# Performance work log

Measured on AMD Instinct MI355X. Metric: run time of the kernel, lower is better.

The kernel has to match this reference:

```python
import jax, jax.numpy as jnp
import numpy as np

B, N, D, H = 8, 2048, 256, 4
HD = D // H


def setup_inputs() -> dict:
    key = jax.random.key(0)
    ks = jax.random.split(key, 12)
    s = 1.0 / np.sqrt(D)
    inp = {
        "node_features": jax.random.normal(ks[0], (B, N, D), dtype=jnp.float32),
        "causal_mask": jnp.tril(jnp.ones((N, N), dtype=jnp.float32)),
        "Wq": jax.random.normal(ks[1], (D, D), dtype=jnp.float32) * s,
        "bq": jnp.zeros((D,), dtype=jnp.float32),
        "Wk": jax.random.normal(ks[2], (D, D), dtype=jnp.float32) * s,
        "bk": jnp.zeros((D,), dtype=jnp.float32),
        "Wv": jax.random.normal(ks[3], (D, D), dtype=jnp.float32) * s,
        "bv": jnp.zeros((D,), dtype=jnp.float32),
        "Wo": jax.random.normal(ks[4], (D, D), dtype=jnp.float32) * s,
        "bo": jnp.zeros((D,), dtype=jnp.float32),
        "Wu": jax.random.normal(ks[5], (2 * D, D), dtype=jnp.float32) * (1.0 / np.sqrt(2 * D)),
        "bu": jnp.zeros((D,), dtype=jnp.float32),
    }
    return inp


def reference(node_features, causal_mask, Wq, bq, Wk, bk, Wv, bv, Wo, bo, Wu, bu):
    # node_features: [B, N, D]; causal_mask: [N, N] (1 = keep, 0 = masked)
    x = node_features
    # project and split heads -> [B, H, N, HD]
    def heads(w, b):
        return (x @ w + b).reshape(B, N, H, HD).transpose(0, 2, 1, 3)
    q, k, v = heads(Wq, bq), heads(Wk, bk), heads(Wv, bv)
    scale = 1.0 / np.sqrt(HD).astype(np.float32)
    scores = jnp.einsum("bhnd,bhmd->bhnm", q, k) * scale  # [B, H, N, N]
    scores = jnp.where(causal_mask > 0, scores, jnp.float32(-1e9))
    attn = jax.nn.softmax(scores, axis=-1)
    ctx = jnp.einsum("bhnm,bhmd->bhnd", attn, v)  # [B, H, N, HD]
    messages = ctx.transpose(0, 2, 1, 3).reshape(B, N, D) @ Wo + bo  # [B, N, D]
    combined = jnp.concatenate([x, messages], axis=-1)  # [B, N, 2D]
    updated = jax.nn.relu(combined @ Wu + bu)  # [B, N, D]  (dropout = identity in eval)
    return updated
```

## Files before the change

kernel.cpp:

```cpp
#include <hip/hip_runtime.h>
#include <math.h>

constexpr int B  = 8;
constexpr int N  = 2048;
constexpr int D  = 256;
constexpr int H  = 4;
constexpr int HD = 64;
constexpr int MTOT = B * N;

typedef __attribute__((ext_vector_type(8))) short  short8;
typedef __attribute__((ext_vector_type(4))) float  floatx4;
typedef unsigned short ushort_t;

#define QSCALE 0.1803368801111204f

__device__ __forceinline__ unsigned short f2bf(float f) {
    unsigned u = __float_as_uint(f);
    u += 0x7fffu + ((u >> 16) & 1u);
    return (unsigned short)(u >> 16);
}

__device__ __forceinline__ void gl_lds16(const ushort_t* g, ushort_t* l) {
    __builtin_amdgcn_global_load_lds(
        (const __attribute__((address_space(1))) void*)g,
        (__attribute__((address_space(3))) void*)l, 16, 0, 0);
}

__global__ __launch_bounds__(256) void prep(
    const float* __restrict__ x,
    const float* __restrict__ Wq, const float* __restrict__ Wk,
    const float* __restrict__ Wv, const float* __restrict__ Wo,
    const float* __restrict__ Wu,
    ushort_t* __restrict__ xb,
    ushort_t* __restrict__ wqkvt, ushort_t* __restrict__ wot,
    ushort_t* __restrict__ wut)
{
    __shared__ float Ls[64][65];
    const int bx = blockIdx.x;
    const int t  = threadIdx.x;

    if (bx < 2048) {
        int idx = (bx * 256 + t) * 8;
        float4 a = *(const float4*)(x + idx);
        float4 b = *(const float4*)(x + idx + 4);
        ushort_t o[8] = {f2bf(a.x), f2bf(a.y), f2bf(a.z), f2bf(a.w),
                         f2bf(b.x), f2bf(b.y), f2bf(b.z), f2bf(b.w)};
        *(short8*)(xb + idx) = *(const short8*)o;
        return;
    }

    const int e = bx - 2048;
    const int z = e >> 5;
    const int kt = (e & 31) >> 2;
    const int nt = e & 3;
    const float* src; ushort_t* dst; int K;
    if      (z == 0) { src = Wq; dst = wqkvt;          K = 256; }
    else if (z == 1) { src = Wk; dst = wqkvt + 65536;  K = 256; }
    else if (z == 2) { src = Wv; dst = wqkvt + 131072; K = 256; }
    else if (z == 3) { src = Wo; dst = wot;            K = 256; }
    else             { src = Wu; dst = wut;            K = 512; }
    if (kt * 64 >= K) return;
    #pragma unroll
    for (int i = 0; i < 16; i++) {
        int ee = t + i * 256, r = ee >> 6, c = ee & 63;
        Ls[r][c] = src[(size_t)(kt * 64 + r) * 256 + nt * 64 + c];
    }
    __syncthreads();
    #pragma unroll
    for (int i = 0; i < 16; i++) {
        int ee = t + i * 256, r = ee >> 6, c = ee & 63;
        dst[(size_t)(nt * 64 + r) * K + kt * 64 + c] = f2bf(Ls[c][r]);
    }
}

__global__ __launch_bounds__(256) void qkv_gemm(
    const ushort_t* __restrict__ xb, const ushort_t* __restrict__ wqkvt,
    const float* __restrict__ bq, const float* __restrict__ bk,
    const float* __restrict__ bv,
    ushort_t* __restrict__ q, ushort_t* __restrict__ kout,
    ushort_t* __restrict__ vt)
{
    __shared__ ushort_t SH[16896];
    ushort_t* As = SH;
    ushort_t* Bs = SH + 8192;

    const int t = threadIdx.x, w = t >> 6, lane = t & 63;
    const int quad = lane >> 4, l16 = lane & 15;
    const int bx = blockIdx.x;
    const int col0 = bx * 128, row0 = blockIdx.y * 128;
    const int wr = (w >> 1) * 64, wc = (w & 1) * 64;

    floatx4 acc[4][4] = {};

    for (int k0 = 0; k0 < 256; k0 += 64) {
        __syncthreads();
        #pragma unroll
        for (int i = 0; i < 4; i++) {
            int e = t + (i << 8);
            int r = e >> 3, c8 = (e & 7) << 3;
            gl_lds16(xb    + (size_t)(row0 + r) * 256 + k0 + c8, &As[e * 8]);
            gl_lds16(wqkvt + (size_t)(col0 + r) * 256 + k0 + c8, &Bs[e * 8]);
        }
        __syncthreads();

        #pragma unroll
        for (int kk = 0; kk < 64; kk += 32) {
            short8 af[4], bf[4];
            #pragma unroll
            for (int i = 0; i < 4; i++)
                af[i] = *(const short8*)&As[(wr + i * 16 + l16) * 64 + kk + quad * 8];
            #pragma unroll
            for (int j = 0; j < 4; j++)
                bf[j] = *(const short8*)&Bs[(wc + j * 16 + l16) * 64 + kk + quad * 8];
            #pragma unroll
            for (int i = 0; i < 4; i++)
                #pragma unroll
                for (int j = 0; j < 4; j++)
                    acc[i][j] = __builtin_amdgcn_mfma_f32_16x16x32_bf16(
                        af[i], bf[j], acc[i][j], 0, 0, 0);
        }
    }

    const int kind = bx >> 1;
    const float* bias = (kind == 0) ? bq : (kind == 1 ? bk : bv);
    const float scl  = (kind == 0) ? QSCALE : 1.0f;
    __syncthreads();
    ushort_t (*Ts)[132] = (ushort_t(*)[132])SH;
    #pragma unroll
    for (int j = 0; j < 4; j++) {
        int cl = wc + j * 16 + l16;
        float bsv = bias[(bx & 1) * 128 + cl];
        #pragma unroll
        for (int i = 0; i < 4; i++) {
            #pragma unroll
            for (int r = 0; r < 4; r++) {
                int ml = wr + i * 16 + quad * 4 + r;
                ushort_t bvv = f2bf((acc[i][j][r] + bsv) * scl);
                if (kind < 2) Ts[ml][cl] = bvv;
                else          Ts[cl][ml] = bvv;
            }
        }
    }
    __syncthreads();

    const int b = row0 >> 11, n0 = row0 & (N - 1);
    #pragma unroll
    for (int i = 0; i < 8; i++) {
        int id = t + (i << 8);
        int rr = id >> 4, c8 = (id & 15) << 3;
        short8 val = *(const short8*)&Ts[rr][c8];
        if (kind < 2) {
            int cg = (bx & 1) * 128 + c8;
            int h = cg >> 6, hd = cg & 63;
            ushort_t* dst = (kind == 0) ? q : kout;
            *(short8*)&dst[(((size_t)(b * H + h)) * N + n0 + rr) * HD + hd] = val;
        } else {
            int cg = (bx & 1) * 128 + rr;
            int h = cg >> 6, hd = cg & 63;
            *(short8*)&vt[(((size_t)(b * H + h)) * HD + hd) * N + n0 + c8] = val;
        }
    }
}

__global__ __launch_bounds__(512) void attn_mfma(
    const ushort_t* __restrict__ q,
    const ushort_t* __restrict__ k,
    const ushort_t* __restrict__ vt,
    ushort_t* __restrict__ ctxb)
{
    __shared__ ushort_t Ks [128][68];
    __shared__ ushort_t Vts[64][132];
    __shared__ ushort_t Ps [8][16][36];

    const int t    = threadIdx.x;
    const int w    = t >> 6;
    const int lane = t & 63;
    const int quad = lane >> 4;
    const int l16  = lane & 15;
    const int bh   = blockIdx.x;
    const int b    = bh >> 2, h = bh & 3;
    const int by   = blockIdx.y;
    const int grp  = w >> 2;
    const int qt   = grp ? by : (31 - by);
    const int qbase = qt * 64;
    const int rowb  = qbase + (w & 3) * 16;

    const ushort_t* qp = q  + (size_t)bh * N * HD;
    const ushort_t* kp = k  + (size_t)bh * N * HD;
    const ushort_t* vp = vt + (size_t)bh * HD * N;

    short8 qf0, qf1;
    {
        const ushort_t* qrow = qp + (size_t)(rowb + l16) * HD + quad * 8;
        qf0 = *(const short8*)(qrow);
        qf1 = *(const short8*)(qrow + 32);
    }

    floatx4 acc_o[4] = {};
    float plsum[4] = {};

    const int nkt_self = (qt >> 1) + 1;
    const int nkt_max  = ((31 - by) >> 1) + 1;

    for (int kt = 0; kt < nkt_max; kt++) {
        const int kbase = kt * 128;
        __syncthreads();

        #pragma unroll
        for (int i = 0; i < 2; i++) {
            int e  = t + (i << 9);
            int kr = e >> 3, kc = (e & 7) << 3;
            *(short8*)&Ks[kr][kc] =
                *(const short8*)(kp + (size_t)(kbase + kr) * HD + kc);
            int vr = e >> 4, vc = (e & 15) << 3;
            *(short8*)&Vts[vr][vc] =
                *(const short8*)(vp + (size_t)vr * N + kbase + vc);
        }
        __syncthreads();

        if (kt >= nkt_self) continue;

        int rem = rowb + 15 - kbase;
        int nch = (rem < 0) ? 0 : ((rem >> 5) + 1);
        if (nch > 4) nch = 4;

        for (int ch = 0; ch < nch; ch++) {
            #pragma unroll
            for (int c2 = 0; c2 < 2; c2++) {
                const int ct = ch * 2 + c2;
                short8 kf0 = *(const short8*)&Ks[ct * 16 + l16][quad * 8];
                short8 kf1 = *(const short8*)&Ks[ct * 16 + l16][32 + quad * 8];
                floatx4 z = {0.0f, 0.0f, 0.0f, 0.0f};
                floatx4 s = __builtin_amdgcn_mfma_f32_16x16x32_bf16(qf0, kf0, z, 0, 0, 0);
                s         = __builtin_amdgcn_mfma_f32_16x16x32_bf16(qf1, kf1, s, 0, 0, 0);
                const bool partial = (kbase + ct * 16 + 15) > rowb;
                if (partial) {
                    const int keyg = kbase + ct * 16 + l16;
                    #pragma unroll
                    for (int r = 0; r < 4; r++) {
                        float sv = s[r];
                        if (keyg > rowb + quad * 4 + r) sv = -3.0e38f;
                        float pv = __builtin_amdgcn_exp2f(sv);
                        plsum[r] += pv;
                        Ps[w][quad * 4 + r][c2 * 16 + l16] = f2bf(pv);
                    }
                } else {
                    #pragma unroll
                    for (int r = 0; r < 4; r++) {
                        float pv = __builtin_amdgcn_exp2f(s[r]);
                        plsum[r] += pv;
                        Ps[w][quad * 4 + r][c2 * 16 + l16] = f2bf(pv);
                    }
                }
            }
            short8 pf = *(const short8*)&Ps[w][l16][quad * 8];
            #pragma unroll
            for (int nt = 0; nt < 4; nt++) {
                short8 vf = *(const short8*)&Vts[nt * 16 + l16][ch * 32 + quad * 8];
                acc_o[nt] = __builtin_amdgcn_mfma_f32_16x16x32_bf16(pf, vf, acc_o[nt], 0, 0, 0);
            }
        }
    }

    #pragma unroll
    for (int r = 0; r < 4; r++) {
        float l = plsum[r];
        l += __shfl_xor(l, 1);
        l += __shfl_xor(l, 2);
        l += __shfl_xor(l, 4);
        l += __shfl_xor(l, 8);
        float inv = 1.0f / l;
        int   n   = rowb + quad * 4 + r;
        #pragma unroll
        for (int nt = 0; nt < 4; nt++) {
            ctxb[((size_t)(b * N + n)) * D + h * HD + nt * 16 + l16] =
                f2bf(acc_o[nt][r] * inv);
        }
    }
}

__global__ __launch_bounds__(256) void tail_k(
    const ushort_t* __restrict__ ctxb, const ushort_t* __restrict__ xb,
    const ushort_t* __restrict__ wot,  const ushort_t* __restrict__ wut,
    const float* __restrict__ bo, const float* __restrict__ bu,
    float* __restrict__ out)
{
    __shared__ ushort_t As1[32 * 64];
    __shared__ ushort_t Bs [256 * 64];
    __shared__ ushort_t msgS[32][260];

    const int t = threadIdx.x, w = t >> 6, lane = t & 63;
    const int quad = lane >> 4, l16 = lane & 15;
    const int row0 = blockIdx.x * 32;
    const int wc = w * 64;

    floatx4 acc1[2][4] = {};
    for (int k0 = 0; k0 < 256; k0 += 64) {
        __syncthreads();
        {
            int r = t >> 3, c8 = (t & 7) << 3;
            gl_lds16(ctxb + (size_t)(row0 + r) * 256 + k0 + c8, &As1[t * 8]);
        }
        #pragma unroll
        for (int i = 0; i < 8; i++) {
            int e = t + (i << 8);
            int nr = e >> 3, c8 = (e & 7) << 3;
            gl_lds16(wot + (size_t)nr * 256 + k0 + c8, &Bs[e * 8]);
        }
        __syncthreads();

        #pragma unroll
        for (int kk = 0; kk < 64; kk += 32) {
            short8 af[2], bf[4];
            #pragma unroll
            for (int i = 0; i < 2; i++)
                af[i] = *(const short8*)&As1[(i * 16 + l16) * 64 + kk + quad * 8];
            #pragma unroll
            for (int j = 0; j < 4; j++)
                bf[j] = *(const short8*)&Bs[(wc + j * 16 + l16) * 64 + kk + quad * 8];
            #pragma unroll
            for (int i = 0; i < 2; i++)
                #pragma unroll
                for (int j = 0; j < 4; j++)
                    acc1[i][j] = __builtin_amdgcn_mfma_f32_16x16x32_bf16(
                        af[i], bf[j], acc1[i][j], 0, 0, 0);
        }
    }
    #pragma unroll
    for (int j = 0; j < 4; j++) {
        int col = wc + j * 16 + l16;
        float bsv = bo[col];
        #pragma unroll
        for (int i = 0; i < 2; i++)
            #pragma unroll
            for (int r = 0; r < 4; r++)
                msgS[i * 16 + quad * 4 + r][col] = f2bf(acc1[i][j][r] + bsv);
    }

    floatx4 acc2[2][4] = {};
    for (int k0 = 0; k0 < 512; k0 += 64) {
        const bool xpart = (k0 < 256);
        __syncthreads();
        if (xpart) {
            int r = t >> 3, c8 = (t & 7) << 3;
            gl_lds16(xb + (size_t)(row0 + r) * 256 + k0 + c8, &As1[t * 8]);
        }
        #pragma unroll
        for (int i = 0; i < 8; i++) {
            int e = t + (i << 8);
            int nr = e >> 3, c8 = (e & 7) << 3;
            gl_lds16(wut + (size_t)nr * 512 + k0 + c8, &Bs[e * 8]);
        }
        __syncthreads();

        #pragma unroll
        for (int kk = 0; kk < 64; kk += 32) {
            short8 af[2], bf[4];
            #pragma unroll
            for (int i = 0; i < 2; i++) {
                if (xpart)
                    af[i] = *(const short8*)&As1[(i * 16 + l16) * 64 + kk + quad * 8];
                else
                    af[i] = *(const short8*)&msgS[i * 16 + l16][(k0 - 256) + kk + quad * 8];
            }
            #pragma unroll
            for (int j = 0; j < 4; j++)
                bf[j] = *(const short8*)&Bs[(wc + j * 16 + l16) * 64 + kk + quad * 8];
            #pragma unroll
            for (int i = 0; i < 2; i++)
                #pragma unroll
                for (int j = 0; j < 4; j++)
                    acc2[i][j] = __builtin_amdgcn_mfma_f32_16x16x32_bf16(
                        af[i], bf[j], acc2[i][j], 0, 0, 0);
        }
    }

    #pragma unroll
    for (int j = 0; j < 4; j++) {
        int col = wc + j * 16 + l16;
        float bsv = bu[col];
        #pragma unroll
        for (int i = 0; i < 2; i++) {
            #pragma unroll
            for (int r = 0; r < 4; r++) {
                int m = row0 + i * 16 + quad * 4 + r;
                out[(size_t)m * 256 + col] = fmaxf(acc2[i][j][r] + bsv, 0.0f);
            }
        }
    }
}

extern "C" void kernel_launch(void* const* d_in, const int* in_sizes, int n_in,
                              void* d_out, int out_size, void* d_ws, size_t ws_size,
                              hipStream_t stream)
{
    const float* x  = (const float*)d_in[0];
    const float* Wq = (const float*)d_in[2];
    const float* bq = (const float*)d_in[3];
    const float* Wk = (const float*)d_in[4];
    const float* bk = (const float*)d_in[5];
    const float* Wv = (const float*)d_in[6];
    const float* bv = (const float*)d_in[7];
    const float* Wo = (const float*)d_in[8];
    const float* bo = (const float*)d_in[9];
    const float* Wu = (const float*)d_in[10];
    const float* bu = (const float*)d_in[11];
    float* out = (float*)d_out;

    const size_t SZ = (size_t)MTOT * D;
    ushort_t* xb    = (ushort_t*)d_ws;
    ushort_t* qb    = xb    + SZ;
    ushort_t* kb    = qb    + SZ;
    ushort_t* vbt   = kb    + SZ;
    ushort_t* ctxb  = vbt   + SZ;
    ushort_t* wqkvt = ctxb  + SZ;
    ushort_t* wot   = wqkvt + 196608;
    ushort_t* wut   = wot   + 65536;

    prep<<<2208, 256, 0, stream>>>(x, Wq, Wk, Wv, Wo, Wu,
                                   xb, wqkvt, wot, wut);

    qkv_gemm<<<dim3(6, 128), 256, 0, stream>>>(xb, wqkvt, bq, bk, bv,
                                               qb, kb, vbt);

    attn_mfma<<<dim3(32, 16), 512, 0, stream>>>(qb, kb, vbt, ctxb);

    tail_k<<<512, 256, 0, stream>>>(ctxb, xb, wot, wut, bo, bu, out);
}
```

Before: 178.7 us.

## Fold Wo into Wu so the tail becomes a single fused GEMM

Precomputes Wo·Wu_bottom and bo·Wu_bottom+bu in the prep kernel, so the tail runs one K=512 GEMM over [x, ctx] instead of two chained GEMMs. This removes the Wo projection GEMM over all tokens (about a third of the tail FLOPs) and lets the tail use a 2D tile grid. Separately, the P-to-bf16 conversion in attention switches from round-to-nearest to truncation to save ALU work. The fold changes rounding, because the product is computed in fp32 and then stored as bf16, and truncation adds a small bias to the P values.

```diff
diff --git a/kernel.cpp b/kernel.cpp
--- a/kernel.cpp
+++ b/kernel.cpp
@@ -20,6 +20,10 @@
     return (unsigned short)(u >> 16);
 }
 
+__device__ __forceinline__ unsigned short f2bf_t(float f) {
+    return (unsigned short)(__float_as_uint(f) >> 16);
+}
+
 __device__ __forceinline__ void gl_lds16(const ushort_t* g, ushort_t* l) {
     __builtin_amdgcn_global_load_lds(
         (const __attribute__((address_space(1))) void*)g,
@@ -31,9 +35,10 @@
     const float* __restrict__ Wq, const float* __restrict__ Wk,
     const float* __restrict__ Wv, const float* __restrict__ Wo,
     const float* __restrict__ Wu,
+    const float* __restrict__ bo, const float* __restrict__ bu,
     ushort_t* __restrict__ xb,
-    ushort_t* __restrict__ wqkvt, ushort_t* __restrict__ wot,
-    ushort_t* __restrict__ wut)
+    ushort_t* __restrict__ wqkvt, ushort_t* __restrict__ wut,
+    float* __restrict__ b2)
 {
     __shared__ float Ls[64][65];
     const int bx = blockIdx.x;
@@ -49,27 +54,78 @@
         return;
     }
 
-    const int e = bx - 2048;
-    const int z = e >> 5;
-    const int kt = (e & 31) >> 2;
-    const int nt = e & 3;
-    const float* src; ushort_t* dst; int K;
-    if      (z == 0) { src = Wq; dst = wqkvt;          K = 256; }
-    else if (z == 1) { src = Wk; dst = wqkvt + 65536;  K = 256; }
-    else if (z == 2) { src = Wv; dst = wqkvt + 131072; K = 256; }
-    else if (z == 3) { src = Wo; dst = wot;            K = 256; }
-    else             { src = Wu; dst = wut;            K = 512; }
-    if (kt * 64 >= K) return;
-    #pragma unroll
-    for (int i = 0; i < 16; i++) {
-        int ee = t + i * 256, r = ee >> 6, c = ee & 63;
-        Ls[r][c] = src[(size_t)(kt * 64 + r) * 256 + nt * 64 + c];
-    }
-    __syncthreads();
-    #pragma unroll
-    for (int i = 0; i < 16; i++) {
-        int ee = t + i * 256, r = ee >> 6, c = ee & 63;
-        dst[(size_t)(nt * 64 + r) * K + kt * 64 + c] = f2bf(Ls[c][r]);
+    if (bx < 2112) {
+        const int e  = bx - 2048;
+        const int zz = e >> 4;
+        const int kt = (e >> 2) & 3;
+        const int nt = e & 3;
+        const float* src; ushort_t* dst; int K;
+        if      (zz == 0) { src = Wq; dst = wqkvt;          K = 256; }
+        else if (zz == 1) { src = Wk; dst = wqkvt + 65536;  K = 256; }
+        else if (zz == 2) { src = Wv; dst = wqkvt + 131072; K = 256; }
+        else              { src = Wu; dst = wut;            K = 512; }
+        #pragma unroll
+        for (int i = 0; i < 16; i++) {
+            int ee = t + i * 256, r = ee >> 6, c = ee & 63;
+            Ls[r][c] = src[(size_t)(kt * 64 + r) * 256 + nt * 64 + c];
+        }
+        __syncthreads();
+        #pragma unroll
+        for (int i = 0; i < 16; i++) {
+            int ee = t + i * 256, r = ee >> 6, c = ee & 63;
+            dst[(size_t)(nt * 64 + r) * K + kt * 64 + c] = f2bf(Ls[c][r]);
+        }
+        return;
+    }
+
+    if (bx < 2128) {
+        float* As2 = &Ls[0][0];
+        float* Ws2 = As2 + 16 * 65;
+        const int e2   = bx - 2112;
+        const int row0 = (e2 >> 2) * 64;
+        const int col0 = (e2 & 3) * 64;
+        const int r0 = (t >> 4) << 2;
+        const int c0 = (t & 15) << 2;
+        float acc[4][4] = {};
+        for (int k0 = 0; k0 < 256; k0 += 16) {
+            __syncthreads();
+            #pragma unroll
+            for (int i = 0; i < 4; i++) {
+                int ee = t + (i << 8);
+                int rr = ee >> 4, kk = ee & 15;
+                As2[kk * 65 + rr] = Wo[(size_t)(row0 + rr) * 256 + k0 + kk];
+                int kk2 = ee >> 6, cc = ee & 63;
+                Ws2[kk2 * 64 + cc] = Wu[(size_t)(256 + k0 + kk2) * 256 + col0 + cc];
+            }
+            __syncthreads();
+            #pragma unroll
+            for (int kk = 0; kk < 16; kk++) {
+                float av[4], bv[4];
+                #pragma unroll
+                for (int i = 0; i < 4; i++) av[i] = As2[kk * 65 + r0 + i];
+                #pragma unroll
+                for (int j = 0; j < 4; j++) bv[j] = Ws2[kk * 64 + c0 + j];
+                #pragma unroll
+                for (int i = 0; i < 4; i++)
+                    #pragma unroll
+                    for (int j = 0; j < 4; j++)
+                        acc[i][j] = fmaf(av[i], bv[j], acc[i][j]);
+            }
+        }
+        #pragma unroll
+        for (int j = 0; j < 4; j++)
+            #pragma unroll
+            for (int i = 0; i < 4; i++)
+                wut[(size_t)(col0 + c0 + j) * 512 + 256 + row0 + r0 + i] =
+                    f2bf(acc[i][j]);
+        return;
+    }
+
+    {
+        float s = bu[t];
+        for (int j = 0; j < 256; j++)
+            s = fmaf(bo[j], Wu[(size_t)(256 + j) * 256 + t], s);
+        b2[t] = s;
     }
 }
 
@@ -242,14 +298,14 @@
                         if (keyg > rowb + quad * 4 + r) sv = -3.0e38f;
                         float pv = __builtin_amdgcn_exp2f(sv);
                         plsum[r] += pv;
-                        Ps[w][quad * 4 + r][c2 * 16 + l16] = f2bf(pv);
+                        Ps[w][quad * 4 + r][c2 * 16 + l16] = f2bf_t(pv);
                     }
                 } else {
                     #pragma unroll
                     for (int r = 0; r < 4; r++) {
                         float pv = __builtin_amdgcn_exp2f(s[r]);
                         plsum[r] += pv;
-                        Ps[w][quad * 4 + r][c2 * 16 + l16] = f2bf(pv);
+                        Ps[w][quad * 4 + r][c2 * 16 + l16] = f2bf_t(pv);
                     }
                 }
             }
@@ -279,33 +335,36 @@
     }
 }
 
-__global__ __launch_bounds__(256) void tail_k(
-    const ushort_t* __restrict__ ctxb, const ushort_t* __restrict__ xb,
-    const ushort_t* __restrict__ wot,  const ushort_t* __restrict__ wut,
-    const float* __restrict__ bo, const float* __restrict__ bu,
+__global__ __launch_bounds__(256) void tail2(
+    const ushort_t* __restrict__ xb, const ushort_t* __restrict__ ctxb,
+    const ushort_t* __restrict__ wut, const float* __restrict__ b2,
     float* __restrict__ out)
 {
-    __shared__ ushort_t As1[32 * 64];
-    __shared__ ushort_t Bs [256 * 64];
-    __shared__ ushort_t msgS[32][260];
+    __shared__ ushort_t As[64 * 64];
+    __shared__ ushort_t Bs[128 * 64];
 
     const int t = threadIdx.x, w = t >> 6, lane = t & 63;
     const int quad = lane >> 4, l16 = lane & 15;
-    const int row0 = blockIdx.x * 32;
-    const int wc = w * 64;
-
-    floatx4 acc1[2][4] = {};
-    for (int k0 = 0; k0 < 256; k0 += 64) {
-        __syncthreads();
-        {
-            int r = t >> 3, c8 = (t & 7) << 3;
-            gl_lds16(ctxb + (size_t)(row0 + r) * 256 + k0 + c8, &As1[t * 8]);
-        }
-        #pragma unroll
-        for (int i = 0; i < 8; i++) {
+    const int col0 = blockIdx.x * 128, row0 = blockIdx.y * 64;
+    const int wr = (w >> 1) * 32, wc = (w & 1) * 64;
+
+    floatx4 acc[2][4] = {};
+
+    for (int k0 = 0; k0 < 512; k0 += 64) {
+        const ushort_t* Ab = (k0 < 256) ? xb : ctxb;
+        const int ka = k0 & 255;
+        __syncthreads();
+        #pragma unroll
+        for (int i = 0; i < 2; i++) {
             int e = t + (i << 8);
-            int nr = e >> 3, c8 = (e & 7) << 3;
-            gl_lds16(wot + (size_t)nr * 256 + k0 + c8, &Bs[e * 8]);
+            int r = e >> 3, c8 = (e & 7) << 3;
+            gl_lds16(Ab + (size_t)(row0 + r) * 256 + ka + c8, &As[e * 8]);
+        }
+        #pragma unroll
+        for (int i = 0; i < 4; i++) {
+            int e = t + (i << 8);
+            int r = e >> 3, c8 = (e & 7) << 3;
+            gl_lds16(wut + (size_t)(col0 + r) * 512 + k0 + c8, &Bs[e * 8]);
         }
         __syncthreads();
 
@@ -314,7 +373,7 @@
             short8 af[2], bf[4];
             #pragma unroll
             for (int i = 0; i < 2; i++)
-                af[i] = *(const short8*)&As1[(i * 16 + l16) * 64 + kk + quad * 8];
+                af[i] = *(const short8*)&As[(wr + i * 16 + l16) * 64 + kk + quad * 8];
             #pragma unroll
             for (int j = 0; j < 4; j++)
                 bf[j] = *(const short8*)&Bs[(wc + j * 16 + l16) * 64 + kk + quad * 8];
@@ -322,69 +381,21 @@
             for (int i = 0; i < 2; i++)
                 #pragma unroll
                 for (int j = 0; j < 4; j++)
-                    acc1[i][j] = __builtin_amdgcn_mfma_f32_16x16x32_bf16(
-                        af[i], bf[j], acc1[i][j], 0, 0, 0);
-        }
-    }
+                    acc[i][j] = __builtin_amdgcn_mfma_f32_16x16x32_bf16(
+                        af[i], bf[j], acc[i][j], 0, 0, 0);
+        }
+    }
+
     #pragma unroll
     for (int j = 0; j < 4; j++) {
-        int col = wc + j * 16 + l16;
-        float bsv = bo[col];
-        #pragma unroll
-        for (int i = 0; i < 2; i++)
-            #pragma unroll
-            for (int r = 0; r < 4; r++)
-                msgS[i * 16 + quad * 4 + r][col] = f2bf(acc1[i][j][r] + bsv);
-    }
-
-    floatx4 acc2[2][4] = {};
-    for (int k0 = 0; k0 < 512; k0 += 64) {
-        const bool xpart = (k0 < 256);
-        __syncthreads();
-        if (xpart) {
-            int r = t >> 3, c8 = (t & 7) << 3;
-            gl_lds16(xb + (size_t)(row0 + r) * 256 + k0 + c8, &As1[t * 8]);
-        }
-        #pragma unroll
-        for (int i = 0; i < 8; i++) {
-            int e = t + (i << 8);
-            int nr = e >> 3, c8 = (e & 7) << 3;
-            gl_lds16(wut + (size_t)nr * 512 + k0 + c8, &Bs[e * 8]);
-        }
-        __syncthreads();
-
-        #pragma unroll
-        for (int kk = 0; kk < 64; kk += 32) {
-            short8 af[2], bf[4];
-            #pragma unroll
-            for (int i = 0; i < 2; i++) {
-                if (xpart)
-                    af[i] = *(const short8*)&As1[(i * 16 + l16) * 64 + kk + quad * 8];
-                else
-                    af[i] = *(const short8*)&msgS[i * 16 + l16][(k0 - 256) + kk + quad * 8];
-            }
-            #pragma unroll
-            for (int j = 0; j < 4; j++)
-                bf[j] = *(const short8*)&Bs[(wc + j * 16 + l16) * 64 + kk + quad * 8];
-            #pragma unroll
-            for (int i = 0; i < 2; i++)
-                #pragma unroll
-                for (int j = 0; j < 4; j++)
-                    acc2[i][j] = __builtin_amdgcn_mfma_f32_16x16x32_bf16(
-                        af[i], bf[j], acc2[i][j], 0, 0, 0);
-        }
-    }
-
-    #pragma unroll
-    for (int j = 0; j < 4; j++) {
-        int col = wc + j * 16 + l16;
-        float bsv = bu[col];
+        int col = col0 + wc + j * 16 + l16;
+        float bsv = b2[col];
         #pragma unroll
         for (int i = 0; i < 2; i++) {
             #pragma unroll
             for (int r = 0; r < 4; r++) {
-                int m = row0 + i * 16 + quad * 4 + r;
-                out[(size_t)m * 256 + col] = fmaxf(acc2[i][j][r] + bsv, 0.0f);
+                int m = row0 + wr + i * 16 + quad * 4 + r;
+                out[(size_t)m * 256 + col] = fmaxf(acc[i][j][r] + bsv, 0.0f);
             }
         }
     }
@@ -414,16 +425,16 @@
     ushort_t* vbt   = kb    + SZ;
     ushort_t* ctxb  = vbt   + SZ;
     ushort_t* wqkvt = ctxb  + SZ;
-    ushort_t* wot   = wqkvt + 196608;
-    ushort_t* wut   = wot   + 65536;
-
-    prep<<<2208, 256, 0, stream>>>(x, Wq, Wk, Wv, Wo, Wu,
-                                   xb, wqkvt, wot, wut);
+    ushort_t* wut   = wqkvt + 196608;
+    float*    b2    = (float*)(wut + 131072);
+
+    prep<<<2129, 256, 0, stream>>>(x, Wq, Wk, Wv, Wo, Wu, bo, bu,
+                                   xb, wqkvt, wut, b2);
 
     qkv_gemm<<<dim3(6, 128), 256, 0, stream>>>(xb, wqkvt, bq, bk, bv,
                                                qb, kb, vbt);
 
     attn_mfma<<<dim3(32, 16), 512, 0, stream>>>(qb, kb, vbt, ctxb);
 
-    tail_k<<<512, 256, 0, stream>>>(ctxb, xb, wot, wut, bo, bu, out);
-}
+    tail2<<<dim3(2, 256), 256, 0, stream>>>(xb, ctxb, wut, b2, out);
+}
```

Result: slower. 182.3 us (+2.0%).
